# Kernel optimization log

Measured on AMD Instinct MI355X. Metric: run time of the kernel, lower is better.

The kernel has to match this reference:

```python
import jax, jax.numpy as jnp
import numpy as np

B = 4096          # batch_size
D = 256           # embedding dim
N = 2 * B
TEMPERATURE = 0.5
GAMMA = 2.0
ALPHA = 0.25


def _negative_indices():
    # Static column indices of negatives per row: all columns except self (i)
    # and the positive partner ((i+B) mod N). Shape (N, N-2).
    idx = []
    for i in range(N):
        partner = (i + B) % N
        cols = [j for j in range(N) if j != i and j != partner]
        idx.append(cols)
    return np.asarray(idx, dtype=np.int32)

_NEG_IDX = jnp.asarray(_negative_indices())


def setup_inputs() -> dict:
    key = jax.random.key(0)
    kx, ky = jax.random.split(key)
    zx = jax.random.normal(kx, (B, D), dtype=jnp.float32)
    zy = jax.random.normal(ky, (B, D), dtype=jnp.float32)
    return {"zx": zx, "zy": zy}


def reference(zx, zy):
    z = jnp.concatenate([zx, zy], axis=0)                    # (N, D)
    zn = z / jnp.linalg.norm(z, axis=1, keepdims=True)       # cosine normalize
    sim = (zn @ zn.T) / TEMPERATURE                          # (N, N)

    sim_xy = jnp.diagonal(sim, offset=B)                     # (B,)
    sim_yx = jnp.diagonal(sim, offset=-B)                    # (B,)
    pos = jnp.concatenate([sim_xy, sim_yx])[:, None]         # (N, 1)
    neg = jnp.take_along_axis(sim, _NEG_IDX, axis=1)         # (N, N-2)

    logits = jnp.concatenate([pos, neg], axis=1)             # (N, N-1)
    # CE with label 0 for every row: -log_softmax(logits)[:, 0]
    ce = jax.nn.logsumexp(logits, axis=1) - logits[:, 0]
    pt = jnp.exp(-ce)
    focal = (1.0 - pt) ** GAMMA * ce
    return (ALPHA * focal).mean()
```

## Files before the change

### kernel.cpp

```cpp
#include <hip/hip_runtime.h>
#include <stdint.h>
#include <stddef.h>


typedef __attribute__((ext_vector_type(8))) short short8;
typedef __attribute__((ext_vector_type(4))) float f32x4;

#define NROWS 8192
#define DDIM 256
#define NBLK 512

__device__ __forceinline__ unsigned short f2bf(float f) {
  unsigned int u = __float_as_uint(f);
  u = (u + 0x7FFFu + ((u >> 16) & 1u)) >> 16;
  return (unsigned short)u;
}

__global__ __launch_bounds__(256) void norm_kernel(const float* __restrict__ zx,
                                                   const float* __restrict__ zy,
                                                   unsigned short* __restrict__ zn,
                                                   unsigned int* __restrict__ counter) {
  if (blockIdx.x == 0 && threadIdx.x == 0) *counter = 0u;
  const int row = blockIdx.x * 4 + (threadIdx.x >> 6);
  const int lane = threadIdx.x & 63;
  const float* src = (row < 4096) ? (zx + (size_t)row * DDIM)
                                  : (zy + (size_t)(row - 4096) * DDIM);
  float4 v = reinterpret_cast<const float4*>(src)[lane];
  float ss = v.x * v.x + v.y * v.y + v.z * v.z + v.w * v.w;
#pragma unroll
  for (int m = 1; m < 64; m <<= 1) ss += __shfl_xor(ss, m);
  const float sc = 1.69864360f * rsqrtf(ss);
  ushort4 o;
  o.x = f2bf(v.x * sc); o.y = f2bf(v.y * sc);
  o.z = f2bf(v.z * sc); o.w = f2bf(v.w * sc);
  reinterpret_cast<ushort4*>(zn + (size_t)row * DDIM)[lane] = o;
}

__global__ __launch_bounds__(256, 2) void simtri_kernel(const unsigned short* __restrict__ zn,
                                                        float* __restrict__ partial,
                                                        float* __restrict__ pos) {
  __shared__ unsigned short smem[2][2][128 * 64];
  __shared__ float stash[5][4][128];
  const int c = (blockIdx.x & 7) * 64 + (blockIdx.x >> 3);
  const int cl = c & 63;
  const int nt = ((cl & 15) == 0) ? 5 : 4;
  const int start = 4 * c + 4 * (c >> 6) + ((cl + 15) >> 4);

  int cp, cq;
  {
    const int j = start / 65, r = start - j * 65;
    if (r <= j) { cp = r; cq = j; } else { cp = r - j - 1; cq = 63 - j; }
  }
  const int p0 = cp, q0 = cq;
  auto advance = [&](int& p, int& q) {
    if (p < q) { ++p; return; }
    p = 0;
    q = (q < 32) ? (63 - q) : (64 - q);
  };

  const int tid = threadIdx.x;
  const int lane = tid & 63;
  const int wid = tid >> 6;
  const int wr = wid >> 1;
  const int wc = wid & 1;
  const int hi = lane >> 4, lo = lane & 15;
  const int sw = lo & 7;

  const f32x4 z4 = {0.f, 0.f, 0.f, 0.f};
  f32x4 acc[4][4];
#pragma unroll
  for (int m = 0; m < 4; ++m)
#pragma unroll
    for (int n = 0; n < 4; ++n) acc[m][n] = z4;

  auto stage_one = [&](int buf, int which, int row0, int k0) {
    unsigned short* lb = &smem[buf][which][0];
#pragma unroll
    for (int j = 0; j < 4; ++j) {
      const int u = j * 256 + tid;
      const int r = u >> 3, ul = u & 7;
      const unsigned short* g =
          zn + (size_t)(row0 + r) * DDIM + k0 + ((ul ^ (r & 7)) << 3);
      unsigned short* l = lb + (size_t)(j * 256 + wid * 64) * 8;
      __builtin_amdgcn_global_load_lds(
          (const __attribute__((address_space(1))) void*)g,
          (__attribute__((address_space(3))) void*)l, 16, 0, 0);
    }
  };
  auto stageT = [&](int buf, int p, int q, int k0) {
    stage_one(buf, 0, p << 7, k0);
    if (p != q) stage_one(buf, 1, q << 7, k0);
  };

  stageT(0, cp, cq, 0);
  __syncthreads();

  int buf = 0;
  for (int i = 0; i < nt; ++i) {
    int np = cp, nq = cq;
    const bool have_next = (i + 1 < nt);
    if (have_next) advance(np, nq);
    const bool isdiag = (cp == cq);
    const bool ispos = (cq == cp + 32);
    const int R0 = cp << 7;

#pragma unroll
    for (int kk = 0; kk < 4; ++kk) {
      if (kk < 3) stageT(buf ^ 1, cp, cq, (kk + 1) * 64);
      else if (have_next) stageT(buf ^ 1, np, nq, 0);
      const unsigned short* A = &smem[buf][0][0];
      const unsigned short* Bm = isdiag ? A : &smem[buf][1][0];
#pragma unroll
      for (int ks = 0; ks < 2; ++ks) {
        short8 af[4], bfr[4];
#pragma unroll
        for (int m = 0; m < 4; ++m)
          af[m] = *reinterpret_cast<const short8*>(
              A + ((wr * 64 + m * 16 + lo) * 64 + (((ks * 4 + hi) ^ sw) << 3)));
#pragma unroll
        for (int n = 0; n < 4; ++n)
          bfr[n] = *reinterpret_cast<const short8*>(
              Bm + ((wc * 64 + n * 16 + lo) * 64 + (((ks * 4 + hi) ^ sw) << 3)));
#pragma unroll
        for (int m = 0; m < 4; ++m)
#pragma unroll
          for (int n = 0; n < 4; ++n)
            acc[m][n] = __builtin_amdgcn_mfma_f32_16x16x32_bf16(af[m], bfr[n], acc[m][n], 0, 0, 0);
      }
      buf ^= 1;
      if (kk < 3) __syncthreads();
    }

    float rsum[4][4];
    float csum[4];
#pragma unroll
    for (int m = 0; m < 4; ++m)
#pragma unroll
      for (int r = 0; r < 4; ++r) rsum[m][r] = 0.f;
#pragma unroll
    for (int n = 0; n < 4; ++n) csum[n] = 0.f;
#pragma unroll
    for (int m = 0; m < 4; ++m)
#pragma unroll
      for (int n = 0; n < 4; ++n)
#pragma unroll
        for (int r = 0; r < 4; ++r) {
          const float e = __builtin_amdgcn_exp2f(acc[m][n][r]);
          rsum[m][r] += e;
          csum[n] += e;
        }
    if ((isdiag || ispos) && (wr == wc)) {
#pragma unroll
      for (int m = 0; m < 4; ++m)
#pragma unroll
        for (int r = 0; r < 4; ++r)
          if (lo == 4 * hi + r) {
            if (isdiag) rsum[m][r] -= __builtin_amdgcn_exp2f(acc[m][m][r]);
            else        pos[R0 + wr * 64 + m * 16 + lo] = acc[m][m][r];
          }
    }
#pragma unroll
    for (int m = 0; m < 4; ++m)
#pragma unroll
      for (int r = 0; r < 4; ++r) {
        float s = rsum[m][r];
        s += __shfl_xor(s, 1); s += __shfl_xor(s, 2);
        s += __shfl_xor(s, 4); s += __shfl_xor(s, 8);
        if (lo == 0) stash[i][wc][wr * 64 + m * 16 + (hi << 2) + r] = s;
      }
    if (!isdiag) {
#pragma unroll
      for (int n = 0; n < 4; ++n) {
        float cs = csum[n];
        cs += __shfl_xor(cs, 16); cs += __shfl_xor(cs, 32);
        if (lane < 16) stash[i][2 + wr][wc * 64 + n * 16 + lane] = cs;
      }
    }

#pragma unroll
    for (int m = 0; m < 4; ++m)
#pragma unroll
      for (int n = 0; n < 4; ++n) acc[m][n] = z4;

    __syncthreads();
    cp = np; cq = nq;
  }

  __syncthreads();
  {
    int fp = p0, fq = q0;
    const int half = tid >> 7;
    const int rr = tid & 127;
    for (int i = 0; i < nt; ++i) {
      partial[(size_t)(fq * 2 + half) * NROWS + fp * 128 + rr] = stash[i][half][rr];
      if (fp != fq)
        partial[(size_t)(fp * 2 + half) * NROWS + fq * 128 + rr] = stash[i][2 + half][rr];
      advance(fp, fq);
    }
  }
}

__global__ __launch_bounds__(256) void d1_kernel(const float* __restrict__ partial,
                                                 const float* __restrict__ pos,
                                                 float* __restrict__ bsum,
                                                 float* __restrict__ out,
                                                 unsigned int* __restrict__ counter) {
  const int row = blockIdx.x * 256 + threadIdx.x;
  float s = 0.f;
#pragma unroll 16
  for (int c = 0; c < 128; ++c) s += partial[(size_t)c * NROWS + row];
  const float L = __log2f(s) - pos[row & 4095];
  const float pt = __builtin_amdgcn_exp2f(-L);
  const float ce = 0.69314718056f * L;
  float f = (1.f - pt) * (1.f - pt) * ce;
#pragma unroll
  for (int m = 1; m < 64; m <<= 1) f += __shfl_xor(f, m);
  __shared__ float wsum[4];
  if ((threadIdx.x & 63) == 0) wsum[threadIdx.x >> 6] = f;
  __syncthreads();
  if (threadIdx.x == 0) {
    bsum[blockIdx.x] = wsum[0] + wsum[1] + wsum[2] + wsum[3];
    __threadfence();
    if (atomicAdd(counter, 1u) == 31u) {
      __threadfence();
      float v = 0.f;
#pragma unroll
      for (int c = 0; c < 32; ++c) v += ((const volatile float*)bsum)[c];
      out[0] = 0.25f * v / 8192.f;
    }
  }
}

extern "C" void kernel_launch(void* const* d_in, const int* in_sizes, int n_in,
                              void* d_out, int out_size, void* d_ws, size_t ws_size,
                              hipStream_t stream) {
  const float* zx = (const float*)d_in[0];
  const float* zy = (const float*)d_in[1];
  float* out = (float*)d_out;

  unsigned short* zn = (unsigned short*)d_ws;
  float* pos = (float*)((char*)d_ws + (size_t)NROWS * DDIM * 2);
  float* partial = pos + 4096;
  float* bsum = partial + (size_t)128 * NROWS;
  unsigned int* counter = (unsigned int*)(bsum + 32);

  norm_kernel<<<2048, 256, 0, stream>>>(zx, zy, zn, counter);
  simtri_kernel<<<NBLK, 256, 0, stream>>>(zn, partial, pos);
  d1_kernel<<<32, 256, 0, stream>>>(partial, pos, bsum, out, counter);
}
```

Baseline: 108.7 us.

## Enlarge sim tiles to 256x256 with 512-thread blocks and explicit pipelining

```diff
diff --git a/kernel.cpp b/kernel.cpp
--- a/kernel.cpp
+++ b/kernel.cpp
@@ -8,7 +8,6 @@
 
 #define NROWS 8192
 #define DDIM 256
-#define NBLK 512
 
 __device__ __forceinline__ unsigned short f2bf(float f) {
   unsigned int u = __float_as_uint(f);
@@ -36,166 +35,204 @@
   reinterpret_cast<ushort4*>(zn + (size_t)row * DDIM)[lane] = o;
 }
 
-__global__ __launch_bounds__(256, 2) void simtri_kernel(const unsigned short* __restrict__ zn,
+__global__ __launch_bounds__(512, 2) void simtri_kernel(const unsigned short* __restrict__ zn,
                                                         float* __restrict__ partial,
                                                         float* __restrict__ pos) {
-  __shared__ unsigned short smem[2][2][128 * 64];
-  __shared__ float stash[5][4][128];
-  const int c = (blockIdx.x & 7) * 64 + (blockIdx.x >> 3);
-  const int cl = c & 63;
-  const int nt = ((cl & 15) == 0) ? 5 : 4;
-  const int start = 4 * c + 4 * (c >> 6) + ((cl + 15) >> 4);
-
-  int cp, cq;
-  {
-    const int j = start / 65, r = start - j * 65;
-    if (r <= j) { cp = r; cq = j; } else { cp = r - j - 1; cq = 63 - j; }
-  }
-  const int p0 = cp, q0 = cq;
-  auto advance = [&](int& p, int& q) {
-    if (p < q) { ++p; return; }
-    p = 0;
-    q = (q < 32) ? (63 - q) : (64 - q);
-  };
+  __shared__ unsigned short smem[2][4][128 * 64];
+  __shared__ float tmp_r[4][256];
+  __shared__ float tmp_c[2][256];
+  __shared__ float stashf[3][2][256];
+
+  const int x = blockIdx.x & 7;
+  const int l = blockIdx.x >> 3;
+  const int nt = (l < 2) ? 3 : 2;
+  int TP[3], TQ[3];
+  for (int i = 0; i < 3; ++i) {
+    const int r = (i == 2) ? (64 + l) : (l + 32 * i);
+    int pc, rr;
+    if (r < 33) { pc = 2 * x;     rr = r; }
+    else        { pc = 2 * x + 1; rr = r - 33; }
+    if (rr <= pc) { TP[i] = rr;          TQ[i] = pc; }
+    else          { TP[i] = rr - pc - 1; TQ[i] = 31 - pc; }
+  }
 
   const int tid = threadIdx.x;
   const int lane = tid & 63;
   const int wid = tid >> 6;
-  const int wr = wid >> 1;
-  const int wc = wid & 1;
+  const int wm = wid >> 2;
+  const int wn = wid & 3;
   const int hi = lane >> 4, lo = lane & 15;
   const int sw = lo & 7;
 
   const f32x4 z4 = {0.f, 0.f, 0.f, 0.f};
-  f32x4 acc[4][4];
-#pragma unroll
-  for (int m = 0; m < 4; ++m)
+  f32x4 acc[8][4];
+#pragma unroll
+  for (int m = 0; m < 8; ++m)
 #pragma unroll
     for (int n = 0; n < 4; ++n) acc[m][n] = z4;
 
-  auto stage_one = [&](int buf, int which, int row0, int k0) {
-    unsigned short* lb = &smem[buf][which][0];
-#pragma unroll
-    for (int j = 0; j < 4; ++j) {
-      const int u = j * 256 + tid;
+  auto stage_half = [&](int b, int slot, int row0, int k0) {
+    unsigned short* lb = &smem[b][slot][0];
+#pragma unroll
+    for (int j = 0; j < 2; ++j) {
+      const int u = j * 512 + tid;
       const int r = u >> 3, ul = u & 7;
       const unsigned short* g =
           zn + (size_t)(row0 + r) * DDIM + k0 + ((ul ^ (r & 7)) << 3);
-      unsigned short* l = lb + (size_t)(j * 256 + wid * 64) * 8;
+      unsigned short* ldst = lb + (size_t)(j * 512 + wid * 64) * 8;
       __builtin_amdgcn_global_load_lds(
           (const __attribute__((address_space(1))) void*)g,
-          (__attribute__((address_space(3))) void*)l, 16, 0, 0);
-    }
-  };
-  auto stageT = [&](int buf, int p, int q, int k0) {
-    stage_one(buf, 0, p << 7, k0);
-    if (p != q) stage_one(buf, 1, q << 7, k0);
-  };
-
-  stageT(0, cp, cq, 0);
-  __syncthreads();
-
-  int buf = 0;
-  for (int i = 0; i < nt; ++i) {
-    int np = cp, nq = cq;
-    const bool have_next = (i + 1 < nt);
-    if (have_next) advance(np, nq);
-    const bool isdiag = (cp == cq);
-    const bool ispos = (cq == cp + 32);
-    const int R0 = cp << 7;
-
-#pragma unroll
-    for (int kk = 0; kk < 4; ++kk) {
-      if (kk < 3) stageT(buf ^ 1, cp, cq, (kk + 1) * 64);
-      else if (have_next) stageT(buf ^ 1, np, nq, 0);
-      const unsigned short* A = &smem[buf][0][0];
-      const unsigned short* Bm = isdiag ? A : &smem[buf][1][0];
-#pragma unroll
-      for (int ks = 0; ks < 2; ++ks) {
-        short8 af[4], bfr[4];
-#pragma unroll
-        for (int m = 0; m < 4; ++m)
-          af[m] = *reinterpret_cast<const short8*>(
-              A + ((wr * 64 + m * 16 + lo) * 64 + (((ks * 4 + hi) ^ sw) << 3)));
+          (__attribute__((address_space(3))) void*)ldst, 16, 0, 0);
+    }
+  };
+  auto stage_kt = [&](int b, int P, int Q, int k0) {
+    stage_half(b, 0, P * 256, k0);
+    stage_half(b, 1, P * 256 + 128, k0);
+    stage_half(b, 2, Q * 256, k0);
+    stage_half(b, 3, Q * 256 + 128, k0);
+  };
+
+  auto consume = [&](int b) {
+    const unsigned short* A0 = &smem[b][wm][0];
+    const unsigned short* B0 = &smem[b][2 + (wn >> 1)][0];
+    const int brbase = (wn & 1) * 64;
+#pragma unroll
+    for (int ks = 0; ks < 2; ++ks) {
+      const int ko = (((ks << 2) + hi) ^ sw) << 3;
+      short8 af[4], bf4[4];
+#pragma unroll
+      for (int n = 0; n < 4; ++n)
+        bf4[n] = *reinterpret_cast<const short8*>(B0 + (brbase + n * 16 + lo) * 64 + ko);
+#pragma unroll
+      for (int m = 0; m < 4; ++m)
+        af[m] = *reinterpret_cast<const short8*>(A0 + (m * 16 + lo) * 64 + ko);
+      __builtin_amdgcn_s_setprio(1);
+#pragma unroll
+      for (int m = 0; m < 4; ++m)
 #pragma unroll
         for (int n = 0; n < 4; ++n)
-          bfr[n] = *reinterpret_cast<const short8*>(
-              Bm + ((wc * 64 + n * 16 + lo) * 64 + (((ks * 4 + hi) ^ sw) << 3)));
-#pragma unroll
-        for (int m = 0; m < 4; ++m)
-#pragma unroll
-          for (int n = 0; n < 4; ++n)
-            acc[m][n] = __builtin_amdgcn_mfma_f32_16x16x32_bf16(af[m], bfr[n], acc[m][n], 0, 0, 0);
-      }
-      buf ^= 1;
-      if (kk < 3) __syncthreads();
-    }
-
-    float rsum[4][4];
-    float csum[4];
-#pragma unroll
-    for (int m = 0; m < 4; ++m)
-#pragma unroll
-      for (int r = 0; r < 4; ++r) rsum[m][r] = 0.f;
-#pragma unroll
-    for (int n = 0; n < 4; ++n) csum[n] = 0.f;
-#pragma unroll
-    for (int m = 0; m < 4; ++m)
+          acc[m][n] = __builtin_amdgcn_mfma_f32_16x16x32_bf16(af[m], bf4[n], acc[m][n], 0, 0, 0);
+      __builtin_amdgcn_s_setprio(0);
+#pragma unroll
+      for (int m = 0; m < 4; ++m)
+        af[m] = *reinterpret_cast<const short8*>(A0 + ((m + 4) * 16 + lo) * 64 + ko);
+      __builtin_amdgcn_s_setprio(1);
+#pragma unroll
+      for (int m = 0; m < 4; ++m)
+#pragma unroll
+        for (int n = 0; n < 4; ++n)
+          acc[m + 4][n] = __builtin_amdgcn_mfma_f32_16x16x32_bf16(af[m], bf4[n], acc[m + 4][n], 0, 0, 0);
+      __builtin_amdgcn_s_setprio(0);
+    }
+  };
+
+  auto epilogue = [&](int si, int tp, int tq) {
+    const bool isdiag = (tp == tq);
+    const bool ispos = (tq == tp + 16);
+    float rowp[8][4];
+    float colp[4] = {0.f, 0.f, 0.f, 0.f};
+#pragma unroll
+    for (int m = 0; m < 8; ++m)
+#pragma unroll
+      for (int v = 0; v < 4; ++v) rowp[m][v] = 0.f;
+#pragma unroll
+    for (int m = 0; m < 8; ++m)
 #pragma unroll
       for (int n = 0; n < 4; ++n)
 #pragma unroll
-        for (int r = 0; r < 4; ++r) {
-          const float e = __builtin_amdgcn_exp2f(acc[m][n][r]);
-          rsum[m][r] += e;
-          csum[n] += e;
+        for (int v = 0; v < 4; ++v) {
+          const float e = __builtin_amdgcn_exp2f(acc[m][n][v]);
+          rowp[m][v] += e;
+          colp[n] += e;
         }
-    if ((isdiag || ispos) && (wr == wc)) {
-#pragma unroll
-      for (int m = 0; m < 4; ++m)
-#pragma unroll
-        for (int r = 0; r < 4; ++r)
-          if (lo == 4 * hi + r) {
-            if (isdiag) rsum[m][r] -= __builtin_amdgcn_exp2f(acc[m][m][r]);
-            else        pos[R0 + wr * 64 + m * 16 + lo] = acc[m][m][r];
+    if (isdiag || ispos) {
+#pragma unroll
+      for (int m = 0; m < 8; ++m)
+#pragma unroll
+        for (int n = 0; n < 4; ++n)
+#pragma unroll
+          for (int v = 0; v < 4; ++v) {
+            const int lr = wm * 128 + m * 16 + (hi << 2) + v;
+            const int lc = wn * 64 + n * 16 + lo;
+            if (lr == lc) {
+              if (isdiag) rowp[m][v] -= __builtin_amdgcn_exp2f(acc[m][n][v]);
+              else        pos[tp * 256 + lr] = acc[m][n][v];
+            }
           }
     }
 #pragma unroll
-    for (int m = 0; m < 4; ++m)
-#pragma unroll
-      for (int r = 0; r < 4; ++r) {
-        float s = rsum[m][r];
+    for (int m = 0; m < 8; ++m)
+#pragma unroll
+      for (int v = 0; v < 4; ++v) {
+        float s = rowp[m][v];
         s += __shfl_xor(s, 1); s += __shfl_xor(s, 2);
         s += __shfl_xor(s, 4); s += __shfl_xor(s, 8);
-        if (lo == 0) stash[i][wc][wr * 64 + m * 16 + (hi << 2) + r] = s;
+        if (lo == 0) tmp_r[wn][wm * 128 + m * 16 + (hi << 2) + v] = s;
       }
-    if (!isdiag) {
-#pragma unroll
-      for (int n = 0; n < 4; ++n) {
-        float cs = csum[n];
-        cs += __shfl_xor(cs, 16); cs += __shfl_xor(cs, 32);
-        if (lane < 16) stash[i][2 + wr][wc * 64 + n * 16 + lane] = cs;
-      }
-    }
-
-#pragma unroll
-    for (int m = 0; m < 4; ++m)
+#pragma unroll
+    for (int n = 0; n < 4; ++n) {
+      float s = colp[n];
+      s += __shfl_xor(s, 16); s += __shfl_xor(s, 32);
+      if (lane < 16) tmp_c[wm][wn * 64 + n * 16 + lo] = s;
+    }
+    __syncthreads();
+    if (tid < 256) {
+      stashf[si][0][tid] = tmp_r[0][tid] + tmp_r[1][tid] + tmp_r[2][tid] + tmp_r[3][tid];
+    } else {
+      const int cc = tid - 256;
+      stashf[si][1][cc] = tmp_c[0][cc] + tmp_c[1][cc];
+    }
+  };
+
+  stage_kt(0, TP[0], TQ[0], 0);
+  stage_kt(1, TP[0], TQ[0], 64);
+
+  for (int i = 0; i < nt; ++i) {
+    const bool hn = (i + 1 < nt);
+    asm volatile("s_waitcnt vmcnt(8)" ::: "memory");
+    __builtin_amdgcn_s_barrier();
+    __builtin_amdgcn_sched_barrier(0);
+    consume(0);
+    __builtin_amdgcn_sched_barrier(0);
+    __builtin_amdgcn_s_barrier();
+    stage_kt(0, TP[i], TQ[i], 128);
+    asm volatile("s_waitcnt vmcnt(8)" ::: "memory");
+    __builtin_amdgcn_s_barrier();
+    __builtin_amdgcn_sched_barrier(0);
+    consume(1);
+    __builtin_amdgcn_sched_barrier(0);
+    __builtin_amdgcn_s_barrier();
+    stage_kt(1, TP[i], TQ[i], 192);
+    asm volatile("s_waitcnt vmcnt(8)" ::: "memory");
+    __builtin_amdgcn_s_barrier();
+    __builtin_amdgcn_sched_barrier(0);
+    consume(0);
+    __builtin_amdgcn_sched_barrier(0);
+    __builtin_amdgcn_s_barrier();
+    if (hn) stage_kt(0, TP[i + 1], TQ[i + 1], 0);
+    if (hn) { asm volatile("s_waitcnt vmcnt(8)" ::: "memory"); }
+    else    { asm volatile("s_waitcnt vmcnt(0)" ::: "memory"); }
+    __builtin_amdgcn_s_barrier();
+    __builtin_amdgcn_sched_barrier(0);
+    consume(1);
+    __builtin_amdgcn_sched_barrier(0);
+    __builtin_amdgcn_s_barrier();
+    if (hn) stage_kt(1, TP[i + 1], TQ[i + 1], 64);
+    epilogue(i, TP[i], TQ[i]);
+#pragma unroll
+    for (int m = 0; m < 8; ++m)
 #pragma unroll
       for (int n = 0; n < 4; ++n) acc[m][n] = z4;
-
-    __syncthreads();
-    cp = np; cq = nq;
-  }
-
-  __syncthreads();
+  }
+
   {
-    int fp = p0, fq = q0;
-    const int half = tid >> 7;
-    const int rr = tid & 127;
+    const int half = tid >> 8;
+    const int rr = tid & 255;
     for (int i = 0; i < nt; ++i) {
-      partial[(size_t)(fq * 2 + half) * NROWS + fp * 128 + rr] = stash[i][half][rr];
-      if (fp != fq)
-        partial[(size_t)(fp * 2 + half) * NROWS + fq * 128 + rr] = stash[i][2 + half][rr];
-      advance(fp, fq);
+      if (half == 0)
+        partial[(size_t)TQ[i] * NROWS + TP[i] * 256 + rr] = stashf[i][0][rr];
+      else if (TP[i] != TQ[i])
+        partial[(size_t)TP[i] * NROWS + TQ[i] * 256 + rr] = stashf[i][1][rr];
     }
   }
 }
@@ -207,8 +244,8 @@
                                                  unsigned int* __restrict__ counter) {
   const int row = blockIdx.x * 256 + threadIdx.x;
   float s = 0.f;
-#pragma unroll 16
-  for (int c = 0; c < 128; ++c) s += partial[(size_t)c * NROWS + row];
+#pragma unroll 8
+  for (int c = 0; c < 32; ++c) s += partial[(size_t)c * NROWS + row];
   const float L = __log2f(s) - pos[row & 4095];
   const float pt = __builtin_amdgcn_exp2f(-L);
   const float ce = 0.69314718056f * L;
@@ -241,10 +278,10 @@
   unsigned short* zn = (unsigned short*)d_ws;
   float* pos = (float*)((char*)d_ws + (size_t)NROWS * DDIM * 2);
   float* partial = pos + 4096;
-  float* bsum = partial + (size_t)128 * NROWS;
+  float* bsum = partial + (size_t)32 * NROWS;
   unsigned int* counter = (unsigned int*)(bsum + 32);
 
   norm_kernel<<<2048, 256, 0, stream>>>(zx, zy, zn, counter);
-  simtri_kernel<<<NBLK, 256, 0, stream>>>(zn, partial, pos);
+  simtri_kernel<<<256, 512, 0, stream>>>(zn, partial, pos);
   d1_kernel<<<32, 256, 0, stream>>>(partial, pos, bsum, out, counter);
 }
```

Result: no change. 110.5 us (+1.6%).
